# Performance work log

Hardware: AMD Instinct MI355X
Metric: run time of the kernel (lower is better)

Reference implementation:

```python
import jax, jax.numpy as jnp
import numpy as np

D_MODEL = 1024
NUM_HEADS = 16
D_K = D_MODEL // NUM_HEADS
MAX_SEQ_LEN = 2048
THETA = 10000.0


def setup_inputs() -> dict:
    key = jax.random.key(0)
    k0, k1, k2, k3, k4 = jax.random.split(key, 5)
    B, S = 2, 2048
    std = (2.0 / (D_MODEL + D_MODEL)) ** 0.5
    # trunc_normal with std=std*std approximated by normal scaled (same distributional scale)
    w = lambda k: (std * std) * jax.random.truncated_normal(k, -3.0 / std, 3.0 / std, (D_MODEL, D_MODEL), jnp.float32)
    return {
        "in_features": jax.random.normal(k0, (B, S, D_MODEL), jnp.float32),
        "token_positions": jnp.arange(S, dtype=jnp.int32),
        "Wq": w(k1), "Wk": w(k2), "Wv": w(k3), "Wo": w(k4),
    }


def _rope(x, token_positions):
    # x: [B, H, S, d_k]; interleaved even/odd rotation
    freq = 1.0 / jnp.power(THETA, jnp.arange(0, D_K, 2, dtype=jnp.float32) / D_K)
    pos = jnp.arange(MAX_SEQ_LEN, dtype=jnp.float32)
    freqs = jnp.outer(pos, freq)                      # [max_seq, d_k/2]
    cos = jnp.cos(freqs)[token_positions]             # [S, d_k/2]
    sin = jnp.sin(freqs)[token_positions]
    even, odd = x[..., 0::2], x[..., 1::2]
    even_out = even * cos - odd * sin
    odd_out = even * sin + odd * cos
    return jnp.stack([even_out, odd_out], axis=-1).reshape(x.shape)


def reference(in_features, token_positions, Wq, Wk, Wv, Wo):
    B, S, _ = in_features.shape
    split = lambda t: t.reshape(B, S, NUM_HEADS, D_K).transpose(0, 2, 1, 3)  # [B,H,S,d_k]
    q = split(in_features @ Wq.T)
    k = split(in_features @ Wk.T)
    v = split(in_features @ Wv.T)
    q = _rope(q, token_positions)
    k = _rope(k, token_positions)
    score = jnp.einsum('bhqd,bhkd->bhqk', q, k) / jnp.sqrt(jnp.float32(D_K))
    mask = jnp.tril(jnp.ones((S, S), dtype=bool))
    score = jnp.where(mask, score, -jnp.inf)
    attn = jax.nn.softmax(score, axis=-1)
    out = jnp.einsum('bhqk,bhkd->bhqd', attn, v)       # [B,H,S,d_k]
    out = out.transpose(0, 2, 1, 3).reshape(B, S, D_MODEL)
    return out @ Wo.T
```

## Files before the change

kernel.cpp:

```cpp
#include <hip/hip_runtime.h>
#include <stdint.h>


typedef unsigned short u16;
typedef __bf16 bf16x8 __attribute__((ext_vector_type(8)));
typedef float f32x4 __attribute__((ext_vector_type(4)));
typedef u16 u16x4 __attribute__((ext_vector_type(4)));

#define LOG2E 1.44269504088896340736f
#define QSCALE (0.125f * LOG2E)

static __device__ __forceinline__ u16 f2bf(float f) {
  __bf16 b = (__bf16)f;
  return __builtin_bit_cast(u16, b);
}

template<bool F32>
static __device__ __forceinline__ bf16x8 load8(const void* p, size_t off) {
  if constexpr (F32) {
    const float* f = (const float*)p + off;
    f32x4 a = *(const f32x4*)f;
    f32x4 b = *(const f32x4*)(f + 4);
    bf16x8 r;
    r[0] = (__bf16)a[0]; r[1] = (__bf16)a[1]; r[2] = (__bf16)a[2]; r[3] = (__bf16)a[3];
    r[4] = (__bf16)b[0]; r[5] = (__bf16)b[1]; r[6] = (__bf16)b[2]; r[7] = (__bf16)b[3];
    return r;
  } else {
    return *(const bf16x8*)((const u16*)p + off);
  }
}

static __device__ __forceinline__ void glds16(const u16* g, u16* l) {
  __builtin_amdgcn_global_load_lds(
      (const __attribute__((address_space(1))) unsigned int*)g,
      (__attribute__((address_space(3))) unsigned int*)l, 16, 0, 0);
}

__global__ void rope_tables_kernel(const int* __restrict__ tp,
                                   float* __restrict__ cosT, float* __restrict__ sinT) {
  int idx = blockIdx.x * 256 + threadIdx.x;
  if (idx >= 2048 * 32) return;
  int s = idx >> 5, i = idx & 31;
  float p = (float)tp[s];
  float freq = powf(10000.0f, -(float)i / 32.0f);
  float ang = p * freq;
  cosT[idx] = cosf(ang);
  sinT[idx] = sinf(ang);
}

__global__ void cvt_bf16_kernel(const float* __restrict__ in,
                                u16* __restrict__ out, int n8) {
  int i = blockIdx.x * 256 + threadIdx.x;
  if (i >= n8) return;
  const float* p = in + (size_t)i * 8;
  f32x4 a = *(const f32x4*)p;
  f32x4 b = *(const f32x4*)(p + 4);
  bf16x8 r;
  r[0] = (__bf16)a[0]; r[1] = (__bf16)a[1]; r[2] = (__bf16)a[2]; r[3] = (__bf16)a[3];
  r[4] = (__bf16)b[0]; r[5] = (__bf16)b[1]; r[6] = (__bf16)b[2]; r[7] = (__bf16)b[3];
  *(bf16x8*)(out + (size_t)i * 8) = r;
}

__global__ void cvt_w_kernel(const float* __restrict__ Wq, const float* __restrict__ Wk,
                             const float* __restrict__ Wv, const float* __restrict__ Wo,
                             u16* __restrict__ out) {
  const int z = blockIdx.z;
  const float* src = (z == 0) ? Wq : (z == 1) ? Wk : (z == 2) ? Wv : Wo;
  u16* dst = out + (size_t)z * 1024 * 1024;
  int i = blockIdx.x * 256 + threadIdx.x;
  const float* p = src + (size_t)i * 8;
  f32x4 a = *(const f32x4*)p;
  f32x4 b = *(const f32x4*)(p + 4);
  bf16x8 r;
  r[0] = (__bf16)a[0]; r[1] = (__bf16)a[1]; r[2] = (__bf16)a[2]; r[3] = (__bf16)a[3];
  r[4] = (__bf16)b[0]; r[5] = (__bf16)b[1]; r[6] = (__bf16)b[2]; r[7] = (__bf16)b[3];
  *(bf16x8*)(dst + (size_t)i * 8) = r;
}

template<bool AF32, bool BF32>
static __device__ __forceinline__ void gemm128_core(
    const void* __restrict__ A, const void* __restrict__ W,
    u16* As, u16* Bs, int m0, int n0, f32x4 (&acc)[4][4]) {
  const int tid = threadIdx.x;
  const int lane = tid & 63;
  const int wave = tid >> 6;
  const int wr = (wave >> 1) * 64, wc = (wave & 1) * 64;
  const int lr = lane & 15, lg = lane >> 4;
  const int srow = tid >> 2;
  const int scol = (tid & 3) * 8;
  for (int k0 = 0; k0 < 1024; k0 += 32) {
    if constexpr (!AF32 && !BF32) {
      const u16* Ab = (const u16*)A;
      const u16* Wb = (const u16*)W;
      __syncthreads();
      glds16(Ab + (size_t)(m0 + srow) * 1024 + k0 + scol, As + tid * 8);
      glds16(Ab + (size_t)(m0 + 64 + srow) * 1024 + k0 + scol, As + 2048 + tid * 8);
      glds16(Wb + (size_t)(n0 + srow) * 1024 + k0 + scol, Bs + tid * 8);
      glds16(Wb + (size_t)(n0 + 64 + srow) * 1024 + k0 + scol, Bs + 2048 + tid * 8);
      __syncthreads();
    } else {
      bf16x8 ta0 = load8<AF32>(A, (size_t)(m0 + srow) * 1024 + k0 + scol);
      bf16x8 ta1 = load8<AF32>(A, (size_t)(m0 + 64 + srow) * 1024 + k0 + scol);
      bf16x8 tb0 = load8<BF32>(W, (size_t)(n0 + srow) * 1024 + k0 + scol);
      bf16x8 tb1 = load8<BF32>(W, (size_t)(n0 + 64 + srow) * 1024 + k0 + scol);
      __syncthreads();
      *(bf16x8*)(As + tid * 8)        = ta0;
      *(bf16x8*)(As + 2048 + tid * 8) = ta1;
      *(bf16x8*)(Bs + tid * 8)        = tb0;
      *(bf16x8*)(Bs + 2048 + tid * 8) = tb1;
      __syncthreads();
    }
    bf16x8 af[4], bfr[4];
#pragma unroll
    for (int i = 0; i < 4; ++i) {
      af[i]  = *(const bf16x8*)(As + (wr + i * 16 + lr) * 32 + lg * 8);
      bfr[i] = *(const bf16x8*)(Bs + (wc + i * 16 + lr) * 32 + lg * 8);
    }
#pragma unroll
    for (int i = 0; i < 4; ++i)
#pragma unroll
      for (int j = 0; j < 4; ++j)
        acc[i][j] = __builtin_amdgcn_mfma_f32_16x16x32_bf16(af[i], bfr[j], acc[i][j], 0, 0, 0);
  }
}

template<bool F32>
__global__ __launch_bounds__(256, 2)
void qkv_gemm_kernel(const void* __restrict__ X,
                     const void* __restrict__ Wq, const void* __restrict__ Wk,
                     const void* __restrict__ Wv,
                     const float* __restrict__ cosT, const float* __restrict__ sinT,
                     u16* __restrict__ Qo, u16* __restrict__ Ko, u16* __restrict__ Vto) {
  __shared__ __align__(16) u16 As[128 * 32];
  __shared__ __align__(16) u16 Bs[128 * 32];
  const int z = blockIdx.z;
  const void* W = (z == 0) ? Wq : ((z == 1) ? Wk : Wv);
  const int m0 = blockIdx.x * 128, n0 = blockIdx.y * 128;
  f32x4 acc[4][4] = {};
  gemm128_core<F32, F32>(X, W, As, Bs, m0, n0, acc);
  const int lane = threadIdx.x & 63, wave = threadIdx.x >> 6;
  const int wr = (wave >> 1) * 64, wc = (wave & 1) * 64;
  const int lr = lane & 15, lg = lane >> 4;
  if (z < 2) {
    u16* dst = z ? Ko : Qo;
    const float qs = z ? 1.0f : QSCALE;
    const int parity = lr & 1;
#pragma unroll
    for (int i = 0; i < 4; ++i) {
      const int rb = m0 + wr + i * 16 + lg * 4;
#pragma unroll
      for (int n = 0; n < 4; ++n) {
        const int c = n0 + wc + n * 16 + lr;
        const int hh = c >> 6, d = c & 63;
        const int ifr = d >> 1;
#pragma unroll
        for (int j = 0; j < 4; ++j) {
          const int r = rb + j;
          const int s = r & 2047;
          float v = acc[i][n][j];
          float p = __shfl_xor(v, 1);
          float cs = cosT[s * 32 + ifr];
          float sn = sinT[s * 32 + ifr];
          float res = parity ? (p * sn + v * cs) : (v * cs - p * sn);
          dst[(((size_t)(r >> 11) * 16 + hh) * 2048 + s) * 64 + d] =
              f2bf(res * qs);
        }
      }
    }
  } else {
#pragma unroll
    for (int i = 0; i < 4; ++i) {
      const int s0 = m0 + wr + i * 16 + lg * 4;
      const int bb = s0 >> 11, ss = s0 & 2047;
#pragma unroll
      for (int n = 0; n < 4; ++n) {
        const int c = n0 + wc + n * 16 + lr;
        const int hh = c >> 6, d = c & 63;
        u16x4 pk;
#pragma unroll
        for (int j = 0; j < 4; ++j) pk[j] = f2bf(acc[i][n][j]);
        *(u16x4*)(Vto + (((size_t)bb * 16 + hh) * 64 + d) * 2048 + ss) = pk;
      }
    }
  }
}

template<bool MASKED>
static __device__ __forceinline__ void attn_tile(
    const u16* kb, const u16* vb, int kv0, int qrow,
    const bf16x8 (&qf)[2], u16* Psw,
    f32x4 (&accO)[4], float& m, float& l, int lr, int lg) {
  f32x4 sacc[4] = {};
#pragma unroll
  for (int n = 0; n < 4; ++n)
#pragma unroll
    for (int kk = 0; kk < 2; ++kk) {
      const int gsw = ((((kk << 2) | lg) ^ (lr & 7)) << 3);
      bf16x8 kf = *(const bf16x8*)&kb[(n * 16 + lr) * 64 + gsw];
      sacc[n] = __builtin_amdgcn_mfma_f32_16x16x32_bf16(kf, qf[kk], sacc[n], 0, 0, 0);
    }
  if (MASKED) {
#pragma unroll
    for (int n = 0; n < 4; ++n)
#pragma unroll
      for (int j = 0; j < 4; ++j) {
        const int c = kv0 + n * 16 + lg * 4 + j;
        if (c > qrow) sacc[n][j] = -1e30f;
      }
  }
  float t0 = fmaxf(fmaxf(sacc[0][0], sacc[0][1]), sacc[0][2]);
  float t1 = fmaxf(fmaxf(sacc[0][3], sacc[1][0]), sacc[1][1]);
  float t2 = fmaxf(fmaxf(sacc[1][2], sacc[1][3]), sacc[2][0]);
  float t3 = fmaxf(fmaxf(sacc[2][1], sacc[2][2]), sacc[2][3]);
  float t4 = fmaxf(fmaxf(sacc[3][0], sacc[3][1]), sacc[3][2]);
  float tm = fmaxf(fmaxf(t0, t1), fmaxf(fmaxf(t2, t3), fmaxf(t4, sacc[3][3])));
  tm = fmaxf(tm, __shfl_xor(tm, 16));
  tm = fmaxf(tm, __shfl_xor(tm, 32));

  float ssum = 0.f;
  u16x4 pk[4];
  if (__all(tm <= m + 8.0f)) {
#pragma unroll
    for (int n = 0; n < 4; ++n)
#pragma unroll
      for (int j = 0; j < 4; ++j) {
        float p = exp2f(sacc[n][j] - m);
        ssum += p;
        pk[n][j] = f2bf(p);
      }
    ssum += __shfl_xor(ssum, 16);
    ssum += __shfl_xor(ssum, 32);
    l += ssum;
  } else {
    const float mn = fmaxf(m, tm);
    const float al = exp2f(m - mn);
    m = mn;
#pragma unroll
    for (int n = 0; n < 4; ++n)
#pragma unroll
      for (int j = 0; j < 4; ++j) {
        float p = exp2f(sacc[n][j] - mn);
        ssum += p;
        pk[n][j] = f2bf(p);
      }
    ssum += __shfl_xor(ssum, 16);
    ssum += __shfl_xor(ssum, 32);
    l = l * al + ssum;
#pragma unroll
    for (int n = 0; n < 4; ++n)
#pragma unroll
      for (int j = 0; j < 4; ++j)
        accO[n][j] *= al;
  }
#pragma unroll
  for (int n = 0; n < 4; ++n) {
    const int g = n * 4 + lg;
    const int off = ((((g >> 1) ^ (lr & 7)) << 3) | ((g & 1) << 2));
    *(u16x4*)&Psw[lr * 64 + off] = pk[n];
  }
#pragma unroll
  for (int kk = 0; kk < 2; ++kk) {
    const int po = (((kk * 4 + lg) ^ (lr & 7)) << 3);
    bf16x8 pb = *(const bf16x8*)&Psw[lr * 64 + po];
#pragma unroll
    for (int db = 0; db < 4; ++db) {
      const int gsw = ((((kk << 2) | lg) ^ (lr & 7)) << 3);
      bf16x8 vf = *(const bf16x8*)&vb[(db * 16 + lr) * 64 + gsw];
      accO[db] = __builtin_amdgcn_mfma_f32_16x16x32_bf16(vf, pb, accO[db], 0, 0, 0);
    }
  }
}

__global__ __launch_bounds__(256, 4)
void flash_attn_kernel(const u16* __restrict__ Q, const u16* __restrict__ K,
                       const u16* __restrict__ Vt, u16* __restrict__ O) {
  __shared__ __align__(16) u16 Klds[2][64 * 64];
  __shared__ __align__(16) u16 Vlds[2][64 * 64];
  __shared__ __align__(16) u16 Ps[4][16 * 64];
  const int bh = blockIdx.x;
  const int qcb = 31 - (int)blockIdx.y;
  const int b = bh >> 4, h = bh & 15;
  const int tid = threadIdx.x;
  const int wv = tid >> 6, lane = tid & 63;
  const int lr = lane & 15, lg = lane >> 4;
  const int qbase = qcb * 64 + wv * 16;
  const int qrow = qbase + lr;
  const size_t hb = (size_t)bh * (2048 * 64);
  const u16* Qh = Q + hb;
  const u16* Kh = K + hb;
  const u16* Vh = Vt + hb;

  const int sgr = ((lane & 7) ^ (lane >> 3)) << 3;
  const int srw = lane >> 3;
  auto STAGE = [&](int kv0, int bufi) {
    u16* kbd = Klds[bufi];
    u16* vbd = Vlds[bufi];
#pragma unroll
    for (int i = 0; i < 2; ++i) {
      const int r = wv * 16 + i * 8;
      glds16(Kh + (size_t)(kv0 + r + srw) * 64 + sgr, kbd + r * 64);
      glds16(Vh + (size_t)(r + srw) * 2048 + kv0 + sgr, vbd + r * 64);
    }
  };

  bf16x8 qf[2];
#pragma unroll
  for (int kk = 0; kk < 2; ++kk)
    qf[kk] = *(const bf16x8*)(Qh + (size_t)qrow * 64 + kk * 32 + lg * 8);

  f32x4 accO[4] = {};
  float m = -1e30f, l = 0.f;

  const int nt = qcb + 1;
  STAGE(0, 0);
  __syncthreads();
  for (int t = 0; t < nt - 1; ++t) {
    STAGE((t + 1) * 64, (t & 1) ^ 1);
    attn_tile<false>(Klds[t & 1], Vlds[t & 1], t * 64, qrow, qf, Ps[wv],
                     accO, m, l, lr, lg);
    __syncthreads();
  }
  attn_tile<true>(Klds[(nt - 1) & 1], Vlds[(nt - 1) & 1], (nt - 1) * 64, qrow,
                  qf, Ps[wv], accO, m, l, lr, lg);

  const float inv = 1.0f / l;
#pragma unroll
  for (int db = 0; db < 4; ++db) {
    u16x4 pk;
#pragma unroll
    for (int j = 0; j < 4; ++j) pk[j] = f2bf(accO[db][j] * inv);
    const int d = db * 16 + lg * 4;
    *(u16x4*)&O[((size_t)(b * 2048 + qrow) * 16 + h) * 64 + d] = pk;
  }
}

template<bool WF32>
__global__ __launch_bounds__(256, 2)
void out_gemm_kernel(const u16* __restrict__ A, const void* __restrict__ W,
                     float* __restrict__ out) {
  __shared__ __align__(16) u16 As[128 * 32];
  __shared__ __align__(16) u16 Bs[128 * 32];
  const int m0 = blockIdx.x * 128, n0 = blockIdx.y * 128;
  f32x4 acc[4][4] = {};
  gemm128_core<false, WF32>(A, W, As, Bs, m0, n0, acc);
  const int lane = threadIdx.x & 63, wave = threadIdx.x >> 6;
  const int wr = (wave >> 1) * 64, wc = (wave & 1) * 64;
  const int lr = lane & 15, lg = lane >> 4;
#pragma unroll
  for (int i = 0; i < 4; ++i)
#pragma unroll
    for (int n = 0; n < 4; ++n) {
      const int c = n0 + wc + n * 16 + lr;
#pragma unroll
      for (int j = 0; j < 4; ++j) {
        const int r = m0 + wr + i * 16 + lg * 4 + j;
        out[(size_t)r * 1024 + c] = acc[i][n][j];
      }
    }
}

extern "C" void kernel_launch(void* const* d_in, const int* in_sizes, int n_in,
                              void* d_out, int out_size, void* d_ws, size_t ws_size,
                              hipStream_t stream) {
  const float* x  = (const float*)d_in[0];
  const int*   tp = (const int*)d_in[1];
  const float* Wq = (const float*)d_in[2];
  const float* Wk = (const float*)d_in[3];
  const float* Wv = (const float*)d_in[4];
  const float* Wo = (const float*)d_in[5];
  float* out = (float*)d_out;
  const int B = in_sizes[0] / (2048 * 1024);
  const size_t xel = (size_t)B * 2048 * 1024;
  const size_t tsz = xel * sizeof(u16);
  const size_t TBL = 2048 * 32 * 2 * sizeof(float);
  u16* Qb = (u16*)d_out;
  u16* Kb = (u16*)((char*)d_out + tsz);
  char* ws = (char*)d_ws;
  u16* Vt = (u16*)(ws);
  u16* Ob = (u16*)(ws + tsz);
  float* cosT = (float*)(ws + 2 * tsz);
  float* sinT = cosT + 2048 * 32;
  u16* Xb  = (u16*)(ws + 2 * tsz + TBL);
  u16* Wb4 = Xb + xel;
  const size_t need = 2 * tsz + TBL + tsz + 4 * (size_t)(1024 * 1024) * sizeof(u16);
  const bool cvt = ws_size >= need;

  rope_tables_kernel<<<dim3(256), dim3(256), 0, stream>>>(tp, cosT, sinT);
  if (cvt) {
    cvt_bf16_kernel<<<dim3((int)(xel / 8 / 256)), dim3(256), 0, stream>>>(x, Xb, (int)(xel / 8));
    cvt_w_kernel<<<dim3(512, 1, 4), dim3(256), 0, stream>>>(Wq, Wk, Wv, Wo, Wb4);
    qkv_gemm_kernel<false><<<dim3(B * 16, 8, 3), dim3(256), 0, stream>>>(
        Xb, Wb4, Wb4 + 1024 * 1024, Wb4 + 2 * 1024 * 1024, cosT, sinT, Qb, Kb, Vt);
  } else {
    qkv_gemm_kernel<true><<<dim3(B * 16, 8, 3), dim3(256), 0, stream>>>(
        x, Wq, Wk, Wv, cosT, sinT, Qb, Kb, Vt);
  }
  flash_attn_kernel<<<dim3(B * 16, 32), dim3(256), 0, stream>>>(Qb, Kb, Vt, Ob);
  if (cvt) {
    out_gemm_kernel<false><<<dim3(B * 16, 8), dim3(256), 0, stream>>>(
        Ob, Wb4 + 3 * 1024 * 1024, out);
  } else {
    out_gemm_kernel<true><<<dim3(B * 16, 8), dim3(256), 0, stream>>>(Ob, Wo, out);
  }
}
```

Before: 120.4 us.

## Widen GEMM K-tile with swizzled LDS and give each attention wave two query strips

The shared GEMM core now stages 64-wide K slices instead of 32, using an XOR-swizzled LDS layout. This halves the number of barrier pairs per K loop and is meant to avoid bank conflicts, at the cost of twice the LDS per block. The flash attention kernel now processes 128 query rows per block, with each wave owning two 16-row strips that share every staged K/V tile. This halves the K/V staging traffic per query. The trade-offs are fewer blocks, more registers per wave, and waves sitting idle on tiles past their causal limit.

```diff
diff --git a/kernel.cpp b/kernel.cpp
--- a/kernel.cpp
+++ b/kernel.cpp
@@ -86,41 +86,49 @@
   const int wave = tid >> 6;
   const int wr = (wave >> 1) * 64, wc = (wave & 1) * 64;
   const int lr = lane & 15, lg = lane >> 4;
-  const int srow = tid >> 2;
-  const int scol = (tid & 3) * 8;
-  for (int k0 = 0; k0 < 1024; k0 += 32) {
+  const int srow = tid >> 3;
+  const int scol = ((tid & 7) ^ (srow & 7)) * 8;
+  for (int k0 = 0; k0 < 1024; k0 += 64) {
     if constexpr (!AF32 && !BF32) {
       const u16* Ab = (const u16*)A;
       const u16* Wb = (const u16*)W;
       __syncthreads();
-      glds16(Ab + (size_t)(m0 + srow) * 1024 + k0 + scol, As + tid * 8);
-      glds16(Ab + (size_t)(m0 + 64 + srow) * 1024 + k0 + scol, As + 2048 + tid * 8);
-      glds16(Wb + (size_t)(n0 + srow) * 1024 + k0 + scol, Bs + tid * 8);
-      glds16(Wb + (size_t)(n0 + 64 + srow) * 1024 + k0 + scol, Bs + 2048 + tid * 8);
+#pragma unroll
+      for (int i = 0; i < 4; ++i) {
+        glds16(Ab + (size_t)(m0 + srow + i * 32) * 1024 + k0 + scol, As + tid * 8 + i * 2048);
+        glds16(Wb + (size_t)(n0 + srow + i * 32) * 1024 + k0 + scol, Bs + tid * 8 + i * 2048);
+      }
       __syncthreads();
     } else {
-      bf16x8 ta0 = load8<AF32>(A, (size_t)(m0 + srow) * 1024 + k0 + scol);
-      bf16x8 ta1 = load8<AF32>(A, (size_t)(m0 + 64 + srow) * 1024 + k0 + scol);
-      bf16x8 tb0 = load8<BF32>(W, (size_t)(n0 + srow) * 1024 + k0 + scol);
-      bf16x8 tb1 = load8<BF32>(W, (size_t)(n0 + 64 + srow) * 1024 + k0 + scol);
+      bf16x8 ta[4], tb[4];
+#pragma unroll
+      for (int i = 0; i < 4; ++i) {
+        ta[i] = load8<AF32>(A, (size_t)(m0 + srow + i * 32) * 1024 + k0 + scol);
+        tb[i] = load8<BF32>(W, (size_t)(n0 + srow + i * 32) * 1024 + k0 + scol);
+      }
       __syncthreads();
-      *(bf16x8*)(As + tid * 8)        = ta0;
-      *(bf16x8*)(As + 2048 + tid * 8) = ta1;
-      *(bf16x8*)(Bs + tid * 8)        = tb0;
-      *(bf16x8*)(Bs + 2048 + tid * 8) = tb1;
+#pragma unroll
+      for (int i = 0; i < 4; ++i) {
+        *(bf16x8*)(As + tid * 8 + i * 2048) = ta[i];
+        *(bf16x8*)(Bs + tid * 8 + i * 2048) = tb[i];
+      }
       __syncthreads();
     }
-    bf16x8 af[4], bfr[4];
-#pragma unroll
-    for (int i = 0; i < 4; ++i) {
-      af[i]  = *(const bf16x8*)(As + (wr + i * 16 + lr) * 32 + lg * 8);
-      bfr[i] = *(const bf16x8*)(Bs + (wc + i * 16 + lr) * 32 + lg * 8);
-    }
-#pragma unroll
-    for (int i = 0; i < 4; ++i)
-#pragma unroll
-      for (int j = 0; j < 4; ++j)
-        acc[i][j] = __builtin_amdgcn_mfma_f32_16x16x32_bf16(af[i], bfr[j], acc[i][j], 0, 0, 0);
+#pragma unroll
+    for (int kk = 0; kk < 2; ++kk) {
+      bf16x8 af[4], bfr[4];
+#pragma unroll
+      for (int i = 0; i < 4; ++i) {
+        const int ga = ((kk * 4 + lg) ^ (lr & 7)) * 8;
+        af[i]  = *(const bf16x8*)(As + (wr + i * 16 + lr) * 64 + ga);
+        bfr[i] = *(const bf16x8*)(Bs + (wc + i * 16 + lr) * 64 + ga);
+      }
+#pragma unroll
+      for (int i = 0; i < 4; ++i)
+#pragma unroll
+        for (int j = 0; j < 4; ++j)
+          acc[i][j] = __builtin_amdgcn_mfma_f32_16x16x32_bf16(af[i], bfr[j], acc[i][j], 0, 0, 0);
+    }
   }
 }
 
@@ -131,8 +139,8 @@
                      const void* __restrict__ Wv,
                      const float* __restrict__ cosT, const float* __restrict__ sinT,
                      u16* __restrict__ Qo, u16* __restrict__ Ko, u16* __restrict__ Vto) {
-  __shared__ __align__(16) u16 As[128 * 32];
-  __shared__ __align__(16) u16 Bs[128 * 32];
+  __shared__ __align__(16) u16 As[128 * 64];
+  __shared__ __align__(16) u16 Bs[128 * 64];
   const int z = blockIdx.z;
   const void* W = (z == 0) ? Wq : ((z == 1) ? Wk : Wv);
   const int m0 = blockIdx.x * 128, n0 = blockIdx.y * 128;
@@ -186,7 +194,7 @@
 }
 
 template<bool MASKED>
-static __device__ __forceinline__ void attn_tile(
+static __device__ __forceinline__ void attn_rs(
     const u16* kb, const u16* vb, int kv0, int qrow,
     const bf16x8 (&qf)[2], u16* Psw,
     f32x4 (&accO)[4], float& m, float& l, int lr, int lg) {
@@ -278,13 +286,14 @@
   __shared__ __align__(16) u16 Vlds[2][64 * 64];
   __shared__ __align__(16) u16 Ps[4][16 * 64];
   const int bh = blockIdx.x;
-  const int qcb = 31 - (int)blockIdx.y;
+  const int qcb = 15 - (int)blockIdx.y;
   const int b = bh >> 4, h = bh & 15;
   const int tid = threadIdx.x;
   const int wv = tid >> 6, lane = tid & 63;
   const int lr = lane & 15, lg = lane >> 4;
-  const int qbase = qcb * 64 + wv * 16;
-  const int qrow = qbase + lr;
+  const int qb32 = qcb * 128 + wv * 32;
+  const int qr0 = qb32 + lr;
+  const int qr1 = qb32 + 16 + lr;
   const size_t hb = (size_t)bh * (2048 * 64);
   const u16* Qh = Q + hb;
   const u16* Kh = K + hb;
@@ -303,34 +312,49 @@
     }
   };
 
-  bf16x8 qf[2];
-#pragma unroll
-  for (int kk = 0; kk < 2; ++kk)
-    qf[kk] = *(const bf16x8*)(Qh + (size_t)qrow * 64 + kk * 32 + lg * 8);
-
-  f32x4 accO[4] = {};
-  float m = -1e30f, l = 0.f;
-
-  const int nt = qcb + 1;
+  bf16x8 qf0[2], qf1[2];
+#pragma unroll
+  for (int kk = 0; kk < 2; ++kk) {
+    qf0[kk] = *(const bf16x8*)(Qh + (size_t)qr0 * 64 + kk * 32 + lg * 8);
+    qf1[kk] = *(const bf16x8*)(Qh + (size_t)qr1 * 64 + kk * 32 + lg * 8);
+  }
+
+  f32x4 accO0[4] = {}, accO1[4] = {};
+  float m0 = -1e30f, l0 = 0.f, m1 = -1e30f, l1 = 0.f;
+
+  const int nt = 2 * qcb + 2;
+  const int ntw = (qb32 >> 6) + 1;
   STAGE(0, 0);
   __syncthreads();
-  for (int t = 0; t < nt - 1; ++t) {
-    STAGE((t + 1) * 64, (t & 1) ^ 1);
-    attn_tile<false>(Klds[t & 1], Vlds[t & 1], t * 64, qrow, qf, Ps[wv],
-                     accO, m, l, lr, lg);
+  for (int t = 0; t < nt; ++t) {
+    if (t + 1 < nt) STAGE((t + 1) * 64, (t & 1) ^ 1);
+    if (t < ntw) {
+      const u16* kb = Klds[t & 1];
+      const u16* vb = Vlds[t & 1];
+      const int kv0 = t * 64;
+      if (t == ntw - 1) {
+        attn_rs<true>(kb, vb, kv0, qr0, qf0, Ps[wv], accO0, m0, l0, lr, lg);
+        attn_rs<true>(kb, vb, kv0, qr1, qf1, Ps[wv], accO1, m1, l1, lr, lg);
+      } else {
+        attn_rs<false>(kb, vb, kv0, qr0, qf0, Ps[wv], accO0, m0, l0, lr, lg);
+        attn_rs<false>(kb, vb, kv0, qr1, qf1, Ps[wv], accO1, m1, l1, lr, lg);
+      }
+    }
     __syncthreads();
   }
-  attn_tile<true>(Klds[(nt - 1) & 1], Vlds[(nt - 1) & 1], (nt - 1) * 64, qrow,
-                  qf, Ps[wv], accO, m, l, lr, lg);
-
-  const float inv = 1.0f / l;
+
+  const float inv0 = 1.0f / l0, inv1 = 1.0f / l1;
 #pragma unroll
   for (int db = 0; db < 4; ++db) {
-    u16x4 pk;
-#pragma unroll
-    for (int j = 0; j < 4; ++j) pk[j] = f2bf(accO[db][j] * inv);
+    u16x4 pk0, pk1;
+#pragma unroll
+    for (int j = 0; j < 4; ++j) {
+      pk0[j] = f2bf(accO0[db][j] * inv0);
+      pk1[j] = f2bf(accO1[db][j] * inv1);
+    }
     const int d = db * 16 + lg * 4;
-    *(u16x4*)&O[((size_t)(b * 2048 + qrow) * 16 + h) * 64 + d] = pk;
+    *(u16x4*)&O[((size_t)(b * 2048 + qr0) * 16 + h) * 64 + d] = pk0;
+    *(u16x4*)&O[((size_t)(b * 2048 + qr1) * 16 + h) * 64 + d] = pk1;
   }
 }
 
@@ -338,8 +362,8 @@
 __global__ __launch_bounds__(256, 2)
 void out_gemm_kernel(const u16* __restrict__ A, const void* __restrict__ W,
                      float* __restrict__ out) {
-  __shared__ __align__(16) u16 As[128 * 32];
-  __shared__ __align__(16) u16 Bs[128 * 32];
+  __shared__ __align__(16) u16 As[128 * 64];
+  __shared__ __align__(16) u16 Bs[128 * 64];
   const int m0 = blockIdx.x * 128, n0 = blockIdx.y * 128;
   f32x4 acc[4][4] = {};
   gemm128_core<false, WF32>(A, W, As, Bs, m0, n0, acc);
@@ -395,7 +419,7 @@
     qkv_gemm_kernel<true><<<dim3(B * 16, 8, 3), dim3(256), 0, stream>>>(
         x, Wq, Wk, Wv, cosT, sinT, Qb, Kb, Vt);
   }
-  flash_attn_kernel<<<dim3(B * 16, 32), dim3(256), 0, stream>>>(Qb, Kb, Vt, Ob);
+  flash_attn_kernel<<<dim3(B * 16, 16), dim3(256), 0, stream>>>(Qb, Kb, Vt, Ob);
   if (cvt) {
     out_gemm_kernel<false><<<dim3(B * 16, 8), dim3(256), 0, stream>>>(
         Ob, Wb4 + 3 * 1024 * 1024, out);
```

Measured after the change: 189.4 us. +57.3%, slower.

## Double GEMM K-tile to 64 with XOR-swizzled LDS and MFMA priority hints

Applied to the files above, without the earlier changes.

The shared GEMM core now stages 64-wide K slices per iteration instead of 32, halving the number of barrier pairs per K loop. LDS tiles are stored with an XOR swizzle of the 16-byte column group by row, which avoids bank conflicts on the fragment reads. Separately, the flash-attention tile raises wave priority around its MFMA blocks with s_setprio. LDS use per GEMM block doubles, which may affect occupancy at the two-block launch bound.

```diff
diff --git a/kernel.cpp b/kernel.cpp
--- a/kernel.cpp
+++ b/kernel.cpp
@@ -86,41 +86,49 @@
   const int wave = tid >> 6;
   const int wr = (wave >> 1) * 64, wc = (wave & 1) * 64;
   const int lr = lane & 15, lg = lane >> 4;
-  const int srow = tid >> 2;
-  const int scol = (tid & 3) * 8;
-  for (int k0 = 0; k0 < 1024; k0 += 32) {
+  const int srow = tid >> 3;
+  const int scol = ((tid & 7) ^ (srow & 7)) * 8;
+  for (int k0 = 0; k0 < 1024; k0 += 64) {
     if constexpr (!AF32 && !BF32) {
       const u16* Ab = (const u16*)A;
       const u16* Wb = (const u16*)W;
       __syncthreads();
-      glds16(Ab + (size_t)(m0 + srow) * 1024 + k0 + scol, As + tid * 8);
-      glds16(Ab + (size_t)(m0 + 64 + srow) * 1024 + k0 + scol, As + 2048 + tid * 8);
-      glds16(Wb + (size_t)(n0 + srow) * 1024 + k0 + scol, Bs + tid * 8);
-      glds16(Wb + (size_t)(n0 + 64 + srow) * 1024 + k0 + scol, Bs + 2048 + tid * 8);
+#pragma unroll
+      for (int i = 0; i < 4; ++i) {
+        glds16(Ab + (size_t)(m0 + srow + i * 32) * 1024 + k0 + scol, As + tid * 8 + i * 2048);
+        glds16(Wb + (size_t)(n0 + srow + i * 32) * 1024 + k0 + scol, Bs + tid * 8 + i * 2048);
+      }
       __syncthreads();
     } else {
-      bf16x8 ta0 = load8<AF32>(A, (size_t)(m0 + srow) * 1024 + k0 + scol);
-      bf16x8 ta1 = load8<AF32>(A, (size_t)(m0 + 64 + srow) * 1024 + k0 + scol);
-      bf16x8 tb0 = load8<BF32>(W, (size_t)(n0 + srow) * 1024 + k0 + scol);
-      bf16x8 tb1 = load8<BF32>(W, (size_t)(n0 + 64 + srow) * 1024 + k0 + scol);
+      bf16x8 ta[4], tb[4];
+#pragma unroll
+      for (int i = 0; i < 4; ++i) {
+        ta[i] = load8<AF32>(A, (size_t)(m0 + srow + i * 32) * 1024 + k0 + scol);
+        tb[i] = load8<BF32>(W, (size_t)(n0 + srow + i * 32) * 1024 + k0 + scol);
+      }
       __syncthreads();
-      *(bf16x8*)(As + tid * 8)        = ta0;
-      *(bf16x8*)(As + 2048 + tid * 8) = ta1;
-      *(bf16x8*)(Bs + tid * 8)        = tb0;
-      *(bf16x8*)(Bs + 2048 + tid * 8) = tb1;
+#pragma unroll
+      for (int i = 0; i < 4; ++i) {
+        *(bf16x8*)(As + tid * 8 + i * 2048) = ta[i];
+        *(bf16x8*)(Bs + tid * 8 + i * 2048) = tb[i];
+      }
       __syncthreads();
     }
-    bf16x8 af[4], bfr[4];
-#pragma unroll
-    for (int i = 0; i < 4; ++i) {
-      af[i]  = *(const bf16x8*)(As + (wr + i * 16 + lr) * 32 + lg * 8);
-      bfr[i] = *(const bf16x8*)(Bs + (wc + i * 16 + lr) * 32 + lg * 8);
-    }
-#pragma unroll
-    for (int i = 0; i < 4; ++i)
-#pragma unroll
-      for (int j = 0; j < 4; ++j)
-        acc[i][j] = __builtin_amdgcn_mfma_f32_16x16x32_bf16(af[i], bfr[j], acc[i][j], 0, 0, 0);
+#pragma unroll
+    for (int kk = 0; kk < 2; ++kk) {
+      bf16x8 af[4], bfr[4];
+#pragma unroll
+      for (int i = 0; i < 4; ++i) {
+        const int ga = ((kk * 4 + lg) ^ (lr & 7)) * 8;
+        af[i]  = *(const bf16x8*)(As + (wr + i * 16 + lr) * 64 + ga);
+        bfr[i] = *(const bf16x8*)(Bs + (wc + i * 16 + lr) * 64 + ga);
+      }
+#pragma unroll
+      for (int i = 0; i < 4; ++i)
+#pragma unroll
+        for (int j = 0; j < 4; ++j)
+          acc[i][j] = __builtin_amdgcn_mfma_f32_16x16x32_bf16(af[i], bfr[j], acc[i][j], 0, 0, 0);
+    }
   }
 }
 
@@ -131,8 +139,8 @@
                      const void* __restrict__ Wv,
                      const float* __restrict__ cosT, const float* __restrict__ sinT,
                      u16* __restrict__ Qo, u16* __restrict__ Ko, u16* __restrict__ Vto) {
-  __shared__ __align__(16) u16 As[128 * 32];
-  __shared__ __align__(16) u16 Bs[128 * 32];
+  __shared__ __align__(16) u16 As[128 * 64];
+  __shared__ __align__(16) u16 Bs[128 * 64];
   const int z = blockIdx.z;
   const void* W = (z == 0) ? Wq : ((z == 1) ? Wk : Wv);
   const int m0 = blockIdx.x * 128, n0 = blockIdx.y * 128;
@@ -191,6 +199,7 @@
     const bf16x8 (&qf)[2], u16* Psw,
     f32x4 (&accO)[4], float& m, float& l, int lr, int lg) {
   f32x4 sacc[4] = {};
+  __builtin_amdgcn_s_setprio(1);
 #pragma unroll
   for (int n = 0; n < 4; ++n)
 #pragma unroll
@@ -199,6 +208,7 @@
       bf16x8 kf = *(const bf16x8*)&kb[(n * 16 + lr) * 64 + gsw];
       sacc[n] = __builtin_amdgcn_mfma_f32_16x16x32_bf16(kf, qf[kk], sacc[n], 0, 0, 0);
     }
+  __builtin_amdgcn_s_setprio(0);
   if (MASKED) {
 #pragma unroll
     for (int n = 0; n < 4; ++n)
@@ -258,6 +268,7 @@
     const int off = ((((g >> 1) ^ (lr & 7)) << 3) | ((g & 1) << 2));
     *(u16x4*)&Psw[lr * 64 + off] = pk[n];
   }
+  __builtin_amdgcn_s_setprio(1);
 #pragma unroll
   for (int kk = 0; kk < 2; ++kk) {
     const int po = (((kk * 4 + lg) ^ (lr & 7)) << 3);
@@ -269,6 +280,7 @@
       accO[db] = __builtin_amdgcn_mfma_f32_16x16x32_bf16(vf, pb, accO[db], 0, 0, 0);
     }
   }
+  __builtin_amdgcn_s_setprio(0);
 }
 
 __global__ __launch_bounds__(256, 4)
@@ -338,8 +350,8 @@
 __global__ __launch_bounds__(256, 2)
 void out_gemm_kernel(const u16* __restrict__ A, const void* __restrict__ W,
                      float* __restrict__ out) {
-  __shared__ __align__(16) u16 As[128 * 32];
-  __shared__ __align__(16) u16 Bs[128 * 32];
+  __shared__ __align__(16) u16 As[128 * 64];
+  __shared__ __align__(16) u16 Bs[128 * 64];
   const int m0 = blockIdx.x * 128, n0 = blockIdx.y * 128;
   f32x4 acc[4][4] = {};
   gemm128_core<false, WF32>(A, W, As, Bs, m0, n0, acc);
```

Result: faster. 114.8 us (-4.6%).
